# Optimization experiments

Measured on AMD Instinct MI355X. Metric: run time of the kernel, lower is better.

## Reference

```python
import jax, jax.numpy as jnp
import numpy as np

N_NODES = 100000
N_EDGES = 1600000
IN_DIM = 128
HID_DIM = 128


def gcn_conv(x, W, b, src, dst, n_nodes):
    # PyG GCNConv: linear (no bias) -> symmetric degree norm with self-loops -> scatter-add -> +bias
    h = x @ W  # [N, H]
    e = src.shape[0]
    deg = jax.ops.segment_sum(jnp.ones((e,), dtype=h.dtype), dst, num_segments=n_nodes) + 1.0  # +1 self-loop
    dinv = deg ** -0.5  # deg >= 1 always
    norm = dinv[src] * dinv[dst]  # [E]
    agg = jax.ops.segment_sum(h[src] * norm[:, None], dst, num_segments=n_nodes)
    agg = agg + h * (dinv * dinv)[:, None]  # self-loop contribution
    return agg + b


def setup_inputs() -> dict:
    key = jax.random.key(0)
    ks = jax.random.split(key, 8)
    x = jax.random.normal(ks[0], (N_NODES, IN_DIM), dtype=jnp.float32)
    edge_index = jax.random.randint(ks[1], (2, N_EDGES), 0, N_NODES, dtype=jnp.int32)
    def glorot(k, fan_in, fan_out):
        lim = np.sqrt(6.0 / (fan_in + fan_out)).astype(np.float32)
        return jax.random.uniform(k, (fan_in, fan_out), dtype=jnp.float32, minval=-lim, maxval=lim)
    W1 = glorot(ks[2], IN_DIM, HID_DIM)
    W2 = glorot(ks[3], HID_DIM, HID_DIM)
    W3 = glorot(ks[4], HID_DIM, HID_DIM)
    b1 = jnp.zeros((HID_DIM,), jnp.float32)
    b2 = jnp.zeros((HID_DIM,), jnp.float32)
    b3 = jnp.zeros((HID_DIM,), jnp.float32)
    return {"x": x, "W1": W1, "b1": b1, "W2": W2, "b2": b2, "W3": W3, "b3": b3,
            "edge_index": edge_index}


def reference(x, W1, b1, W2, b2, W3, b3, edge_index):
    src, dst = edge_index[0], edge_index[1]
    n = x.shape[0]
    z = jax.nn.relu(gcn_conv(x, W1, b1, src, dst, n))
    z = jax.nn.relu(gcn_conv(z, W2, b2, src, dst, n))
    z = gcn_conv(z, W3, b3, src, dst, n)
    # edge dot-product decode on the same edge set
    logits = jnp.sum(z[src] * z[dst], axis=1)  # [E]
    return jax.nn.sigmoid(logits)
```

## Files before the change

kernel.cpp:

```cpp
#include <hip/hip_runtime.h>
#include <math.h>

#define NN 100000
#define NE 1600000
#define DIM 128
#define SCHUNK 1024
#define NBK 391
#define ECH 4096

typedef unsigned short u16;
typedef unsigned int u32;
typedef __attribute__((ext_vector_type(8))) short bf16x8;
typedef __attribute__((ext_vector_type(4))) float f32x4;

__device__ inline u16 f2bf(float f) {
  union { float f; u32 u; } v; v.f = f;
  u32 r = v.u + 0x7FFF + ((v.u >> 16) & 1);
  return (u16)(r >> 16);
}
__device__ inline float bflo(u32 u) { union { u32 u; float f; } v; v.u = u << 16; return v.f; }
__device__ inline float bfhi(u32 u) { union { u32 u; float f; } v; v.u = u & 0xFFFF0000u; return v.f; }
__device__ inline float sigm(float x) { return 1.0f / (1.0f + expf(-x)); }

__global__ void k_deg(const int* __restrict__ dst, int* __restrict__ deg) {
  int i = blockIdx.x * blockDim.x + threadIdx.x;
  if (i < NE) atomicAdd(&deg[dst[i]], 1);
}

__global__ void k_scan1(const int* __restrict__ deg, int* __restrict__ bsum) {
  __shared__ int sd[256];
  int t = threadIdx.x;
  int base = blockIdx.x * SCHUNK + t * 4;
  int s = 0;
#pragma unroll
  for (int j = 0; j < 4; ++j) { int idx = base + j; if (idx < NN) s += deg[idx]; }
  sd[t] = s; __syncthreads();
  for (int off = 128; off > 0; off >>= 1) {
    if (t < off) sd[t] += sd[t + off];
    __syncthreads();
  }
  if (t == 0) bsum[blockIdx.x] = sd[0];
}

__global__ void k_scan2(int* __restrict__ bsum, int nb) {
  __shared__ int sd[128];
  int t = threadIdx.x;
  int v = (t < nb) ? bsum[t] : 0;
  sd[t] = v; __syncthreads();
  for (int off = 1; off < 128; off <<= 1) {
    int x = (t >= off) ? sd[t - off] : 0;
    __syncthreads();
    sd[t] += x;
    __syncthreads();
  }
  if (t < nb) bsum[t] = sd[t] - v;
}

__global__ void k_scan3(const int* __restrict__ deg, const int* __restrict__ bsum,
                        int* __restrict__ offs, float* __restrict__ dinv) {
  __shared__ int ts[256];
  int t = threadIdx.x;
  int base = blockIdx.x * SCHUNK + t * 4;
  int v[4]; int loc = 0;
#pragma unroll
  for (int j = 0; j < 4; ++j) { int idx = base + j; v[j] = (idx < NN) ? deg[idx] : 0; loc += v[j]; }
  ts[t] = loc; __syncthreads();
  for (int off = 1; off < 256; off <<= 1) {
    int x = (t >= off) ? ts[t - off] : 0;
    __syncthreads();
    ts[t] += x;
    __syncthreads();
  }
  int run = bsum[blockIdx.x] + ts[t] - loc;
#pragma unroll
  for (int j = 0; j < 4; ++j) {
    int idx = base + j;
    if (idx < NN) {
      offs[idx] = run;
      dinv[idx] = rsqrtf((float)v[j] + 1.0f);
    }
    run += v[j];
  }
}

__launch_bounds__(256)
__global__ void k_bucket(const int* __restrict__ src, const int* __restrict__ dst,
                         const int* __restrict__ offs, int* __restrict__ bcur,
                         uint2* __restrict__ bstage) {
  __shared__ int cnt[512];
  __shared__ int bl[512];
  __shared__ int gb[512];
  __shared__ int tmp[256];
  __shared__ uint2 st[ECH];
  int t = threadIdx.x;
  int e0 = blockIdx.x * ECH;
  cnt[t] = 0; cnt[t + 256] = 0;
  __syncthreads();
  int b_[16], r_[16]; u32 s_[16], y_[16];
#pragma unroll
  for (int k = 0; k < 16; ++k) {
    int i = e0 + k * 256 + t;
    b_[k] = -1;
    if (i < NE) {
      int d = dst[i];
      int bb = d >> 8;
      b_[k] = bb;
      s_[k] = (u32)src[i];
      y_[k] = ((u32)(d & 255) << 21) | (u32)i;
      r_[k] = atomicAdd(&cnt[bb], 1);
    }
  }
  __syncthreads();
  int c0 = cnt[2 * t], c1 = cnt[2 * t + 1];
  tmp[t] = c0 + c1;
  __syncthreads();
  for (int off = 1; off < 256; off <<= 1) {
    int v = (t >= off) ? tmp[t - off] : 0;
    __syncthreads();
    tmp[t] += v;
    __syncthreads();
  }
  int excl = tmp[t] - (c0 + c1);
  bl[2 * t] = excl; bl[2 * t + 1] = excl + c0;
  __syncthreads();
#pragma unroll
  for (int k = 0; k < 16; ++k)
    if (b_[k] >= 0) st[bl[b_[k]] + r_[k]] = make_uint2(s_[k], y_[k]);
  for (int b = t; b < 512; b += 256) {
    int n = cnt[b];
    gb[b] = (n > 0) ? atomicAdd(&bcur[b], n) : 0;
  }
  __syncthreads();
  for (int b = t; b < 512; b += 256) {
    int n = cnt[b];
    if (n > 0) {
      uint2* dp = bstage + offs[b << 8] + gb[b];
      const uint2* sp = st + bl[b];
      for (int j = 0; j < n; ++j) dp[j] = sp[j];
    }
  }
}

__launch_bounds__(256)
__global__ void k_fillb(const uint2* __restrict__ bstage, const int* __restrict__ offs,
                        int* __restrict__ csr_src, int* __restrict__ csr_dst,
                        int* __restrict__ csr_eid) {
  __shared__ int curl[256];
  int t = threadIdx.x;
  int b = blockIdx.x;
  int nb0 = b << 8;
  curl[t] = 0;
  __syncthreads();
  int sbase = offs[nb0];
  int send = (b == NBK - 1) ? NE : offs[nb0 + 256];
  for (int j = sbase + t; j < send; j += 256) {
    uint2 e = bstage[j];
    int dl = e.y >> 21;
    int eid = e.y & 0x1FFFFF;
    int pos = offs[nb0 + dl] + atomicAdd(&curl[dl], 1);
    csr_src[pos] = (int)e.x;
    csr_dst[pos] = nb0 + dl;
    csr_eid[pos] = eid;
  }
}

__global__ void k_tobf(const float* __restrict__ in, u16* __restrict__ out, int n4) {
  int i = blockIdx.x * blockDim.x + threadIdx.x;
  if (i < n4) {
    float4 v = ((const float4*)in)[i];
    ushort4 o;
    o.x = f2bf(v.x); o.y = f2bf(v.y); o.z = f2bf(v.z); o.w = f2bf(v.w);
    ((ushort4*)out)[i] = o;
  }
}

__global__ void k_pack3(const float* __restrict__ W1, const float* __restrict__ W2,
                        const float* __restrict__ W3, u16* __restrict__ Wp1,
                        u16* __restrict__ Wp2, u16* __restrict__ Wp3) {
  int gid = blockIdx.x * blockDim.x + threadIdx.x;
  int which = gid >> 14;
  int tid = gid & 16383;
  const float* W = which == 0 ? W1 : (which == 1 ? W2 : W3);
  u16* Wp = which == 0 ? Wp1 : (which == 1 ? Wp2 : Wp3);
  int b = tid & 7, j = (tid >> 3) & 15, kb = (tid >> 7) & 3, ks = (tid >> 9) & 3, ct = tid >> 11;
  int k = ks * 32 + kb * 8 + b, col = ct * 16 + j;
  Wp[tid] = f2bf(W[k * 128 + col]);
}

__launch_bounds__(256)
__global__ void k_gemm(const u16* __restrict__ Xb, const u16* __restrict__ Wp,
                       const float* __restrict__ dinv, u16* __restrict__ hp) {
  __shared__ u16 wl[16384];
  __shared__ u16 ctile[4][2048];
  int t = threadIdx.x;
  int w = t >> 6, l = t & 63;
  int row0 = blockIdx.x * 64;
  int rbase = row0 + w * 16;

#pragma unroll
  for (int i = 0; i < 8; ++i) {
    int off = (i * 256 + t) * 8;
    *(uint4*)&wl[off] = *(const uint4*)&Wp[off];
  }
  __syncthreads();

  int arow = rbase + (l & 15);
  arow = arow < NN ? arow : NN - 1;
  const u16* abase = Xb + (size_t)arow * DIM + (l >> 4) * 8;
  bf16x8 a[4];
#pragma unroll
  for (int ks = 0; ks < 4; ++ks) a[ks] = *(const bf16x8*)(abase + ks * 32);

  f32x4 acc[8];
#pragma unroll
  for (int ct = 0; ct < 8; ++ct) {
    acc[ct] = (f32x4){0.f, 0.f, 0.f, 0.f};
#pragma unroll
    for (int ks = 0; ks < 4; ++ks) {
      bf16x8 bfr = *(const bf16x8*)&wl[ct * 2048 + ks * 512 + (l >> 4) * 128 + (l & 15) * 8];
      acc[ct] = __builtin_amdgcn_mfma_f32_16x16x32_bf16(a[ks], bfr, acc[ct], 0, 0, 0);
    }
  }

  float dv[4];
#pragma unroll
  for (int v = 0; v < 4; ++v) {
    int rr = rbase + (l >> 4) * 4 + v;
    dv[v] = dinv[rr < NN ? rr : NN - 1];
  }
  u16* ct_lds = ctile[w];
#pragma unroll
  for (int ct = 0; ct < 8; ++ct) {
#pragma unroll
    for (int v = 0; v < 4; ++v) {
      int row = (l >> 4) * 4 + v;
      ct_lds[row * DIM + ct * 16 + (l & 15)] = f2bf(dv[v] * acc[ct][v]);
    }
  }
  __syncthreads();
#pragma unroll
  for (int rr = 0; rr < 4; ++rr) {
    int row = rr * 4 + (l >> 4);
    int grow = rbase + row;
    if (grow < NN)
      *(uint4*)&hp[(size_t)grow * DIM + (l & 15) * 8] =
          *(const uint4*)&ct_lds[row * DIM + (l & 15) * 8];
  }
}

__launch_bounds__(256)
__global__ void k_agg(const u16* __restrict__ hp, const int* __restrict__ csr_src,
                      const int* __restrict__ offs, const int* __restrict__ deg,
                      const float* __restrict__ dinv, const float* __restrict__ bias,
                      u16* __restrict__ outb, int relu) {
  int t = threadIdx.x;
  int g = t >> 5, l = t & 31;
  int n = blockIdx.x * 8 + g;
  float dn = dinv[n];
  int s = offs[n], cnt = deg[n];
  const uint2* hp2 = (const uint2*)hp;
  float a0 = 0.f, a1 = 0.f, a2 = 0.f, a3 = 0.f;
  int i = 0;
  for (; i + 8 <= cnt; i += 8) {
    int u[8];
#pragma unroll
    for (int k = 0; k < 8; ++k) u[k] = csr_src[s + i + k];
    uint2 v[8];
#pragma unroll
    for (int k = 0; k < 8; ++k) v[k] = hp2[(size_t)u[k] * 32 + l];
#pragma unroll
    for (int k = 0; k < 8; ++k) {
      a0 += bflo(v[k].x); a1 += bfhi(v[k].x); a2 += bflo(v[k].y); a3 += bfhi(v[k].y);
    }
  }
  for (; i + 4 <= cnt; i += 4) {
    int u[4];
#pragma unroll
    for (int k = 0; k < 4; ++k) u[k] = csr_src[s + i + k];
    uint2 v[4];
#pragma unroll
    for (int k = 0; k < 4; ++k) v[k] = hp2[(size_t)u[k] * 32 + l];
#pragma unroll
    for (int k = 0; k < 4; ++k) {
      a0 += bflo(v[k].x); a1 += bfhi(v[k].x); a2 += bflo(v[k].y); a3 += bfhi(v[k].y);
    }
  }
  for (; i < cnt; ++i) {
    int u = csr_src[s + i];
    uint2 v = hp2[(size_t)u * 32 + l];
    a0 += bflo(v.x); a1 += bfhi(v.x); a2 += bflo(v.y); a3 += bfhi(v.y);
  }
  uint2 sv = hp2[(size_t)n * 32 + l];
  float4 bb = ((const float4*)bias)[l];
  float r0 = dn * (a0 + bflo(sv.x)) + bb.x;
  float r1 = dn * (a1 + bfhi(sv.x)) + bb.y;
  float r2 = dn * (a2 + bflo(sv.y)) + bb.z;
  float r3 = dn * (a3 + bfhi(sv.y)) + bb.w;
  if (relu) {
    r0 = fmaxf(r0, 0.f); r1 = fmaxf(r1, 0.f);
    r2 = fmaxf(r2, 0.f); r3 = fmaxf(r3, 0.f);
  }
  ushort4 o; o.x = f2bf(r0); o.y = f2bf(r1); o.z = f2bf(r2); o.w = f2bf(r3);
  *(ushort4*)&outb[(size_t)n * DIM + l * 4] = o;
}

__launch_bounds__(256)
__global__ void k_decode_mfma(const u16* __restrict__ z, const int* __restrict__ csr_src,
                              const int* __restrict__ csr_dst, const int* __restrict__ csr_eid,
                              float* __restrict__ out) {
  int l = threadIdx.x & 63;
  int wid = blockIdx.x * 4 + (threadIdx.x >> 6);
  int r = l & 15, g = l >> 4;
  int tile0 = wid * 8;
  for (int tt = 0; tt < 8; ++tt) {
    int p0 = (tile0 + tt) * 16;
    int e = p0 + r;
    int s = csr_src[e];
    int d = csr_dst[e];
    int dprev = __shfl(d, (l & 48) | ((r - 1) & 15));
    unsigned long long bm = __ballot(r > 0 && d != dprev);
    u32 m16 = (u32)(bm >> (l & 48)) & 0xFFFFu;
    u32 m = m16; int rc = 0;
    for (int j = 0; j < r; ++j) {
      if (!m) break;
      rc = __ffs(m) - 1;
      m &= m - 1;
    }
    int dget = __shfl(d, (l & 48) | rc);
    const bf16x8* za = (const bf16x8*)(z + (size_t)s * DIM + g * 8);
    const bf16x8* zc = (const bf16x8*)(z + (size_t)dget * DIM + g * 8);
    f32x4 acc = (f32x4){0.f, 0.f, 0.f, 0.f};
#pragma unroll
    for (int ks = 0; ks < 4; ++ks)
      acc = __builtin_amdgcn_mfma_f32_16x16x32_bf16(za[ks * 4], zc[ks * 4], acc, 0, 0, 0);
#pragma unroll
    for (int reg = 0; reg < 4; ++reg) {
      int rr = g * 4 + reg;
      int colr = __popc(m16 & ((2u << rr) - 1));
      if (colr == r) out[csr_eid[p0 + rr]] = sigm(acc[reg]);
    }
  }
}

extern "C" void kernel_launch(void* const* d_in, const int* in_sizes, int n_in,
                              void* d_out, int out_size, void* d_ws, size_t ws_size,
                              hipStream_t stream) {
  const float* x  = (const float*)d_in[0];
  const float* W1 = (const float*)d_in[1];
  const float* b1 = (const float*)d_in[2];
  const float* W2 = (const float*)d_in[3];
  const float* b2 = (const float*)d_in[4];
  const float* W3 = (const float*)d_in[5];
  const float* b3 = (const float*)d_in[6];
  const int*   ei = (const int*)d_in[7];
  const int* src = ei;
  const int* dst = ei + NE;
  float* out = (float*)d_out;

  char* w = (char*)d_ws;
  size_t p = 0;
  auto alloc = [&](size_t bytes) -> void* {
    void* r = w + p;
    p += (bytes + 255) & ~(size_t)255;
    return r;
  };
  int*   deg     = (int*)alloc((size_t)NN * 4);
  int*   offs    = (int*)alloc((size_t)NN * 4);
  float* dinv    = (float*)alloc((size_t)NN * 4);
  int*   bsum    = (int*)alloc(1024);
  int*   bcur    = (int*)alloc(512 * 4);
  uint2* bstage  = (uint2*)alloc((size_t)NE * 8);
  int*   csr_src = (int*)alloc((size_t)NE * 4);
  int*   csr_dst = (int*)alloc((size_t)NE * 4);
  int*   csr_eid = (int*)alloc((size_t)NE * 4);
  u16*   Xb      = (u16*)alloc((size_t)NN * DIM * 2);
  u16*   hp      = (u16*)alloc((size_t)NN * DIM * 2);
  u16*   hb      = (u16*)alloc((size_t)NN * DIM * 2);
  u16*   Wp1     = (u16*)alloc(16384 * 2);
  u16*   Wp2     = (u16*)alloc(16384 * 2);
  u16*   Wp3     = (u16*)alloc(16384 * 2);
  (void)in_sizes; (void)n_in; (void)out_size; (void)ws_size;

  hipMemsetAsync(deg, 0, (size_t)NN * 4, stream);
  hipMemsetAsync(bcur, 0, 512 * 4, stream);

  k_deg<<<(NE + 255) / 256, 256, 0, stream>>>(dst, deg);
  int nb = (NN + SCHUNK - 1) / SCHUNK;
  k_scan1<<<nb, 256, 0, stream>>>(deg, bsum);
  k_scan2<<<1, 128, 0, stream>>>(bsum, nb);
  k_scan3<<<nb, 256, 0, stream>>>(deg, bsum, offs, dinv);

  int cb = (NE + ECH - 1) / ECH;
  k_bucket<<<cb, 256, 0, stream>>>(src, dst, offs, bcur, bstage);
  k_fillb<<<NBK, 256, 0, stream>>>(bstage, offs, csr_src, csr_dst, csr_eid);

  k_tobf<<<(NN * DIM / 4 + 255) / 256, 256, 0, stream>>>(x, Xb, NN * DIM / 4);
  k_pack3<<<192, 256, 0, stream>>>(W1, W2, W3, Wp1, Wp2, Wp3);

  int gb = (NN + 63) / 64;
  k_gemm<<<gb, 256, 0, stream>>>(Xb, Wp1, dinv, hp);
  k_agg <<<NN / 8, 256, 0, stream>>>(hp, csr_src, offs, deg, dinv, b1, hb, 1);
  k_gemm<<<gb, 256, 0, stream>>>(hb, Wp2, dinv, hp);
  k_agg <<<NN / 8, 256, 0, stream>>>(hp, csr_src, offs, deg, dinv, b2, hb, 1);
  k_gemm<<<gb, 256, 0, stream>>>(hb, Wp3, dinv, hp);
  k_agg <<<NN / 8, 256, 0, stream>>>(hp, csr_src, offs, deg, dinv, b3, hb, 0);

  k_decode_mfma<<<3125, 256, 0, stream>>>(hb, csr_src, csr_dst, csr_eid, out);
}
```

Baseline: 461.0 us.

## Fuse aggregation with next-layer GEMM and fold input bf16 conversion into GEMM

Merges each ReLU aggregation with the following linear transform in one kernel. The aggregated tile is staged in swizzled LDS and fed straight to MFMA, so the intermediate activation round-trip and two launches disappear. The first GEMM now reads fp32 input and converts to bf16 in registers, removing the separate conversion kernel. The decode drops the dst-dedup shuffle logic and uses the MFMA diagonal per edge, trading dst row reuse for simpler control. Weights in the fused kernel are read from global memory instead of LDS.

```diff
diff --git a/kernel.cpp b/kernel.cpp
--- a/kernel.cpp
+++ b/kernel.cpp
@@ -161,16 +161,6 @@
     csr_src[pos] = (int)e.x;
     csr_dst[pos] = nb0 + dl;
     csr_eid[pos] = eid;
-  }
-}
-
-__global__ void k_tobf(const float* __restrict__ in, u16* __restrict__ out, int n4) {
-  int i = blockIdx.x * blockDim.x + threadIdx.x;
-  if (i < n4) {
-    float4 v = ((const float4*)in)[i];
-    ushort4 o;
-    o.x = f2bf(v.x); o.y = f2bf(v.y); o.z = f2bf(v.z); o.w = f2bf(v.w);
-    ((ushort4*)out)[i] = o;
   }
 }
 
@@ -188,8 +178,8 @@
 }
 
 __launch_bounds__(256)
-__global__ void k_gemm(const u16* __restrict__ Xb, const u16* __restrict__ Wp,
-                       const float* __restrict__ dinv, u16* __restrict__ hp) {
+__global__ void k_gemm1(const float* __restrict__ X, const u16* __restrict__ Wp,
+                        const float* __restrict__ dinv, u16* __restrict__ hp) {
   __shared__ u16 wl[16384];
   __shared__ u16 ctile[4][2048];
   int t = threadIdx.x;
@@ -206,10 +196,19 @@
 
   int arow = rbase + (l & 15);
   arow = arow < NN ? arow : NN - 1;
-  const u16* abase = Xb + (size_t)arow * DIM + (l >> 4) * 8;
+  const float* ab = X + (size_t)arow * DIM + (l >> 4) * 8;
   bf16x8 a[4];
 #pragma unroll
-  for (int ks = 0; ks < 4; ++ks) a[ks] = *(const bf16x8*)(abase + ks * 32);
+  for (int ks = 0; ks < 4; ++ks) {
+    float4 f0 = *(const float4*)(ab + ks * 32);
+    float4 f1 = *(const float4*)(ab + ks * 32 + 4);
+    bf16x8 aa;
+    aa[0] = (short)f2bf(f0.x); aa[1] = (short)f2bf(f0.y);
+    aa[2] = (short)f2bf(f0.z); aa[3] = (short)f2bf(f0.w);
+    aa[4] = (short)f2bf(f1.x); aa[5] = (short)f2bf(f1.y);
+    aa[6] = (short)f2bf(f1.z); aa[7] = (short)f2bf(f1.w);
+    a[ks] = aa;
+  }
 
   f32x4 acc[8];
 #pragma unroll
@@ -249,10 +248,119 @@
 }
 
 __launch_bounds__(256)
+__global__ void k_fused(const u16* __restrict__ hp, const int* __restrict__ csr_src,
+                        const int* __restrict__ offs, const int* __restrict__ deg,
+                        const float* __restrict__ dinv, const float* __restrict__ bias,
+                        const u16* __restrict__ Wp, u16* __restrict__ hpo) {
+  __shared__ u16 atile[8192];
+  int t = threadIdx.x;
+  int row0 = blockIdx.x * 64;
+
+  {
+    int g = t >> 5, l = t & 31;
+    const uint2* hp2 = (const uint2*)hp;
+    float4 bb = ((const float4*)bias)[l];
+    for (int pass = 0; pass < 8; ++pass) {
+      int row = pass * 8 + g;
+      int n = row0 + row;
+      int nn = n < NN ? n : NN - 1;
+      float dn = dinv[nn];
+      int s = offs[nn], cnt = deg[nn];
+      float a0 = 0.f, a1 = 0.f, a2 = 0.f, a3 = 0.f;
+      int i = 0;
+      for (; i + 8 <= cnt; i += 8) {
+        int u[8];
+#pragma unroll
+        for (int k = 0; k < 8; ++k) u[k] = csr_src[s + i + k];
+        uint2 v[8];
+#pragma unroll
+        for (int k = 0; k < 8; ++k) v[k] = hp2[(size_t)u[k] * 32 + l];
+#pragma unroll
+        for (int k = 0; k < 8; ++k) {
+          a0 += bflo(v[k].x); a1 += bfhi(v[k].x); a2 += bflo(v[k].y); a3 += bfhi(v[k].y);
+        }
+      }
+      for (; i + 4 <= cnt; i += 4) {
+        int u[4];
+#pragma unroll
+        for (int k = 0; k < 4; ++k) u[k] = csr_src[s + i + k];
+        uint2 v[4];
+#pragma unroll
+        for (int k = 0; k < 4; ++k) v[k] = hp2[(size_t)u[k] * 32 + l];
+#pragma unroll
+        for (int k = 0; k < 4; ++k) {
+          a0 += bflo(v[k].x); a1 += bfhi(v[k].x); a2 += bflo(v[k].y); a3 += bfhi(v[k].y);
+        }
+      }
+      for (; i < cnt; ++i) {
+        int u = csr_src[s + i];
+        uint2 v = hp2[(size_t)u * 32 + l];
+        a0 += bflo(v.x); a1 += bfhi(v.x); a2 += bflo(v.y); a3 += bfhi(v.y);
+      }
+      uint2 sv = hp2[(size_t)nn * 32 + l];
+      float r0 = fmaxf(dn * (a0 + bflo(sv.x)) + bb.x, 0.f);
+      float r1 = fmaxf(dn * (a1 + bfhi(sv.x)) + bb.y, 0.f);
+      float r2 = fmaxf(dn * (a2 + bflo(sv.y)) + bb.z, 0.f);
+      float r3 = fmaxf(dn * (a3 + bfhi(sv.y)) + bb.w, 0.f);
+      ushort4 o; o.x = f2bf(r0); o.y = f2bf(r1); o.z = f2bf(r2); o.w = f2bf(r3);
+      int byte = row * 256 + ((l * 8) ^ ((row & 7) << 4));
+      *(ushort4*)((char*)atile + byte) = o;
+    }
+  }
+  __syncthreads();
+
+  int w = t >> 6, l = t & 63;
+  int rbase = row0 + w * 16;
+  int arow = w * 16 + (l & 15);
+  bf16x8 a[4];
+#pragma unroll
+  for (int ks = 0; ks < 4; ++ks) {
+    int cb = ((l >> 4) * 16 + ks * 64) ^ ((arow & 7) << 4);
+    a[ks] = *(const bf16x8*)((const char*)atile + arow * 256 + cb);
+  }
+  f32x4 acc[8];
+#pragma unroll
+  for (int ct = 0; ct < 8; ++ct) {
+    acc[ct] = (f32x4){0.f, 0.f, 0.f, 0.f};
+#pragma unroll
+    for (int ks = 0; ks < 4; ++ks) {
+      bf16x8 bfr = *(const bf16x8*)&Wp[ct * 2048 + ks * 512 + (l >> 4) * 128 + (l & 15) * 8];
+      acc[ct] = __builtin_amdgcn_mfma_f32_16x16x32_bf16(a[ks], bfr, acc[ct], 0, 0, 0);
+    }
+  }
+  __syncthreads();
+
+  float dv[4];
+#pragma unroll
+  for (int v = 0; v < 4; ++v) {
+    int rr = rbase + (l >> 4) * 4 + v;
+    dv[v] = dinv[rr < NN ? rr : NN - 1];
+  }
+  u16* ct_lds = atile + w * 2048;
+#pragma unroll
+  for (int ct = 0; ct < 8; ++ct) {
+#pragma unroll
+    for (int v = 0; v < 4; ++v) {
+      int row = (l >> 4) * 4 + v;
+      ct_lds[row * DIM + ct * 16 + (l & 15)] = f2bf(dv[v] * acc[ct][v]);
+    }
+  }
+  __syncthreads();
+#pragma unroll
+  for (int rr = 0; rr < 4; ++rr) {
+    int row = rr * 4 + (l >> 4);
+    int grow = rbase + row;
+    if (grow < NN)
+      *(uint4*)&hpo[(size_t)grow * DIM + (l & 15) * 8] =
+          *(const uint4*)&ct_lds[row * DIM + (l & 15) * 8];
+  }
+}
+
+__launch_bounds__(256)
 __global__ void k_agg(const u16* __restrict__ hp, const int* __restrict__ csr_src,
                       const int* __restrict__ offs, const int* __restrict__ deg,
                       const float* __restrict__ dinv, const float* __restrict__ bias,
-                      u16* __restrict__ outb, int relu) {
+                      u16* __restrict__ outb) {
   int t = threadIdx.x;
   int g = t >> 5, l = t & 31;
   int n = blockIdx.x * 8 + g;
@@ -296,10 +404,6 @@
   float r1 = dn * (a1 + bfhi(sv.x)) + bb.y;
   float r2 = dn * (a2 + bflo(sv.y)) + bb.z;
   float r3 = dn * (a3 + bfhi(sv.y)) + bb.w;
-  if (relu) {
-    r0 = fmaxf(r0, 0.f); r1 = fmaxf(r1, 0.f);
-    r2 = fmaxf(r2, 0.f); r3 = fmaxf(r3, 0.f);
-  }
   ushort4 o; o.x = f2bf(r0); o.y = f2bf(r1); o.z = f2bf(r2); o.w = f2bf(r3);
   *(ushort4*)&outb[(size_t)n * DIM + l * 4] = o;
 }
@@ -314,31 +418,16 @@
   int tile0 = wid * 8;
   for (int tt = 0; tt < 8; ++tt) {
     int p0 = (tile0 + tt) * 16;
-    int e = p0 + r;
-    int s = csr_src[e];
-    int d = csr_dst[e];
-    int dprev = __shfl(d, (l & 48) | ((r - 1) & 15));
-    unsigned long long bm = __ballot(r > 0 && d != dprev);
-    u32 m16 = (u32)(bm >> (l & 48)) & 0xFFFFu;
-    u32 m = m16; int rc = 0;
-    for (int j = 0; j < r; ++j) {
-      if (!m) break;
-      rc = __ffs(m) - 1;
-      m &= m - 1;
-    }
-    int dget = __shfl(d, (l & 48) | rc);
+    int s = csr_src[p0 + r];
+    int d = csr_dst[p0 + r];
+    int e = csr_eid[p0 + r];
     const bf16x8* za = (const bf16x8*)(z + (size_t)s * DIM + g * 8);
-    const bf16x8* zc = (const bf16x8*)(z + (size_t)dget * DIM + g * 8);
+    const bf16x8* zb = (const bf16x8*)(z + (size_t)d * DIM + g * 8);
     f32x4 acc = (f32x4){0.f, 0.f, 0.f, 0.f};
 #pragma unroll
     for (int ks = 0; ks < 4; ++ks)
-      acc = __builtin_amdgcn_mfma_f32_16x16x32_bf16(za[ks * 4], zc[ks * 4], acc, 0, 0, 0);
-#pragma unroll
-    for (int reg = 0; reg < 4; ++reg) {
-      int rr = g * 4 + reg;
-      int colr = __popc(m16 & ((2u << rr) - 1));
-      if (colr == r) out[csr_eid[p0 + rr]] = sigm(acc[reg]);
-    }
+      acc = __builtin_amdgcn_mfma_f32_16x16x32_bf16(za[ks * 4], zb[ks * 4], acc, 0, 0, 0);
+    if ((r >> 2) == g) out[e] = sigm(acc[r & 3]);
   }
 }
 
@@ -373,9 +462,9 @@
   int*   csr_src = (int*)alloc((size_t)NE * 4);
   int*   csr_dst = (int*)alloc((size_t)NE * 4);
   int*   csr_eid = (int*)alloc((size_t)NE * 4);
-  u16*   Xb      = (u16*)alloc((size_t)NN * DIM * 2);
   u16*   hp      = (u16*)alloc((size_t)NN * DIM * 2);
   u16*   hb      = (u16*)alloc((size_t)NN * DIM * 2);
+  u16*   zb      = (u16*)alloc((size_t)NN * DIM * 2);
   u16*   Wp1     = (u16*)alloc(16384 * 2);
   u16*   Wp2     = (u16*)alloc(16384 * 2);
   u16*   Wp3     = (u16*)alloc(16384 * 2);
@@ -394,16 +483,12 @@
   k_bucket<<<cb, 256, 0, stream>>>(src, dst, offs, bcur, bstage);
   k_fillb<<<NBK, 256, 0, stream>>>(bstage, offs, csr_src, csr_dst, csr_eid);
 
-  k_tobf<<<(NN * DIM / 4 + 255) / 256, 256, 0, stream>>>(x, Xb, NN * DIM / 4);
   k_pack3<<<192, 256, 0, stream>>>(W1, W2, W3, Wp1, Wp2, Wp3);
 
   int gb = (NN + 63) / 64;
-  k_gemm<<<gb, 256, 0, stream>>>(Xb, Wp1, dinv, hp);
-  k_agg <<<NN / 8, 256, 0, stream>>>(hp, csr_src, offs, deg, dinv, b1, hb, 1);
-  k_gemm<<<gb, 256, 0, stream>>>(hb, Wp2, dinv, hp);
-  k_agg <<<NN / 8, 256, 0, stream>>>(hp, csr_src, offs, deg, dinv, b2, hb, 1);
-  k_gemm<<<gb, 256, 0, stream>>>(hb, Wp3, dinv, hp);
-  k_agg <<<NN / 8, 256, 0, stream>>>(hp, csr_src, offs, deg, dinv, b3, hb, 0);
-
-  k_decode_mfma<<<3125, 256, 0, stream>>>(hb, csr_src, csr_dst, csr_eid, out);
-}
+  k_gemm1<<<gb, 256, 0, stream>>>(x, Wp1, dinv, hp);
+  k_fused<<<gb, 256, 0, stream>>>(hp, csr_src, offs, deg, dinv, b1, Wp2, hb);
+  k_fused<<<gb, 256, 0, stream>>>(hb, csr_src, offs, deg, dinv, b2, Wp3, hp);
+  k_agg <<<NN / 8, 256, 0, stream>>>(hp, csr_src, offs, deg, dinv, b3, zb);
+  k_decode_mfma<<<3125, 256, 0, stream>>>(zb, csr_src, csr_dst, csr_eid, out);
+}
```

Result: slower. 478.4 us (+3.8%).
